# Kernel tuning notes

Measured on AMD Instinct MI355X. Metric: run time of the kernel, lower is better.

## Reference

```python
import jax, jax.numpy as jnp
import numpy as np
from itertools import product

B, D, H, W_, C = 2, 64, 64, 64, 96
OUT = 192  # c_multiplier * dim
EPS = 1e-5


def setup_inputs() -> dict:
    key = jax.random.key(0)
    k1, k2 = jax.random.split(key)
    x = jax.random.normal(k1, (B, D, H, W_, C), dtype=jnp.float32)
    ln_w = jnp.ones((8 * C,), dtype=jnp.float32)
    ln_b = jnp.zeros((8 * C,), dtype=jnp.float32)
    W = jax.random.normal(k2, (OUT, 8 * C), dtype=jnp.float32) * 0.02
    return {"x": x, "ln_w": ln_w, "ln_b": ln_b, "W": W}


def reference(x, ln_w, ln_b, W):
    # strided patch gather + concat: order matches itertools.product over (0,1)^3
    parts = [x[:, s0::2, s1::2, s2::2, :] for s0, s1, s2 in product((0, 1), repeat=3)]
    y = jnp.concatenate(parts, axis=-1)  # [B, D/2, H/2, W/2, 8C]
    # LayerNorm over last dim
    mu = jnp.mean(y, axis=-1, keepdims=True)
    var = jnp.mean(jnp.square(y - mu), axis=-1, keepdims=True)
    y = (y - mu) * jax.lax.rsqrt(var + EPS) * ln_w + ln_b
    # linear reduction (bias=False); torch Linear weight is [out, in]
    return jnp.einsum('bdhwc,oc->bdhwo', y, W)
```

## Files before the change

kernel.cpp:

```cpp
#include <hip/hip_runtime.h>
#include <stdint.h>

#define C_IN   96
#define KIN    768
#define NOUT   192
#define MTILE  32
#define LDK    776
#define EPS    1e-5f

typedef __bf16 bf16x8 __attribute__((ext_vector_type(8)));
typedef float  f32x4  __attribute__((ext_vector_type(4)));

static __device__ __forceinline__ unsigned int f2bf(float f) {
    union { float f; unsigned int u; } v; v.f = f;
    return (v.u + 0x7fffu + ((v.u >> 16) & 1u)) >> 16;
}
static __device__ __forceinline__ float bf2f(unsigned int s) {
    union { unsigned int u; float f; } v; v.u = s << 16;
    return v.f;
}
static __device__ __forceinline__ unsigned int normpack(unsigned int p, float mu, float rs) {
    float lo = (bf2f(p & 0xffffu) - mu) * rs;
    float hi = (bf2f(p >> 16)     - mu) * rs;
    return f2bf(lo) | (f2bf(hi) << 16);
}

__global__ __launch_bounds__(256) void prep_kernel(
    const float* __restrict__ W, const float* __restrict__ lnw,
    const float* __restrict__ lnb, unsigned short* __restrict__ Wb,
    float* __restrict__ bias)
{
    int o = blockIdx.x;
    int tid = threadIdx.x;
    float part = 0.f;
    for (int c = tid; c < KIN; c += 256) {
        float w = W[(size_t)o * KIN + c];
        Wb[(size_t)o * KIN + c] = (unsigned short)f2bf(w * lnw[c]);
        part += w * lnb[c];
    }
    #pragma unroll
    for (int m = 32; m >= 1; m >>= 1) part += __shfl_xor(part, m, 64);
    __shared__ float red[4];
    if ((tid & 63) == 0) red[tid >> 6] = part;
    __syncthreads();
    if (tid == 0) bias[o] = red[0] + red[1] + red[2] + red[3];
}

__global__ __launch_bounds__(256) void merge_kernel(
    const float* __restrict__ x, const unsigned short* __restrict__ Wb,
    const float* __restrict__ bias, float* __restrict__ out)
{
    __shared__ unsigned short ylds[MTILE * LDK];
    __shared__ float muL[MTILE], rsL[MTILE];

    const int tid   = threadIdx.x;
    const int tbase = blockIdx.x * MTILE;
    const int bh = blockIdx.x;
    const int h  = bh & 31;
    const int d  = (bh >> 5) & 31;
    const int b  = bh >> 10;

    const int tk = tid >> 3;
    const int i  = tid & 7;
    float sum = 0.f, sq = 0.f;
    #pragma unroll
    for (int g = 0; g < 8; ++g) {
        const int s0 = g >> 2, s1 = (g >> 1) & 1, s2 = g & 1;
        const float* src = x +
            ((size_t)((b * 64 + 2 * d + s0) * 64 + (2 * h + s1)) * 64 + (2 * tk + s2)) * C_IN;
        #pragma unroll
        for (int jj = 0; jj < 3; ++jj) {
            const int c4 = i + jj * 8;
            float4 v = *(const float4*)(src + c4 * 4);
            sum += v.x + v.y + v.z + v.w;
            sq  += v.x * v.x + v.y * v.y + v.z * v.z + v.w * v.w;
            uint2 p;
            p.x = f2bf(v.x) | (f2bf(v.y) << 16);
            p.y = f2bf(v.z) | (f2bf(v.w) << 16);
            *(uint2*)&ylds[tk * LDK + g * 96 + c4 * 4] = p;
        }
    }
    #pragma unroll
    for (int m = 4; m >= 1; m >>= 1) {
        sum += __shfl_xor(sum, m, 8);
        sq  += __shfl_xor(sq,  m, 8);
    }
    if (i == 0) {
        float mean = sum * (1.f / 768.f);
        float var  = sq * (1.f / 768.f) - mean * mean;
        muL[tk] = mean;
        rsL[tk] = rsqrtf(var + EPS);
    }
    __syncthreads();

    {
        const float mu = muL[tk], rs = rsL[tk];
        unsigned short* row = &ylds[tk * LDK + i * 96];
        #pragma unroll
        for (int jj = 0; jj < 12; ++jj) {
            uint4 u = *(const uint4*)(row + jj * 8);
            u.x = normpack(u.x, mu, rs);
            u.y = normpack(u.y, mu, rs);
            u.z = normpack(u.z, mu, rs);
            u.w = normpack(u.w, mu, rs);
            *(uint4*)(row + jj * 8) = u;
        }
    }
    __syncthreads();

    const int wv    = tid >> 6;
    const int l     = tid & 63;
    const int l15   = l & 15;
    const int quad  = l >> 4;
    const int nbase = wv * 48;
    const int koff  = quad * 8;

    f32x4 acc[2][3];
    #pragma unroll
    for (int mt = 0; mt < 2; ++mt)
        #pragma unroll
        for (int nt = 0; nt < 3; ++nt)
            acc[mt][nt] = (f32x4){0.f, 0.f, 0.f, 0.f};

    const unsigned short* arow0 = &ylds[(l15)      * LDK + koff];
    const unsigned short* arow1 = &ylds[(16 + l15) * LDK + koff];
    const unsigned short* brow0 = Wb + (size_t)(nbase +  0 + l15) * KIN + koff;
    const unsigned short* brow1 = Wb + (size_t)(nbase + 16 + l15) * KIN + koff;
    const unsigned short* brow2 = Wb + (size_t)(nbase + 32 + l15) * KIN + koff;

    #pragma unroll
    for (int kk = 0; kk < 24; ++kk) {
        const int k = kk * 32;
        bf16x8 a0 = *(const bf16x8*)(arow0 + k);
        bf16x8 a1 = *(const bf16x8*)(arow1 + k);
        bf16x8 b0 = *(const bf16x8*)(brow0 + k);
        bf16x8 b1 = *(const bf16x8*)(brow1 + k);
        bf16x8 b2 = *(const bf16x8*)(brow2 + k);
        acc[0][0] = __builtin_amdgcn_mfma_f32_16x16x32_bf16(a0, b0, acc[0][0], 0, 0, 0);
        acc[0][1] = __builtin_amdgcn_mfma_f32_16x16x32_bf16(a0, b1, acc[0][1], 0, 0, 0);
        acc[0][2] = __builtin_amdgcn_mfma_f32_16x16x32_bf16(a0, b2, acc[0][2], 0, 0, 0);
        acc[1][0] = __builtin_amdgcn_mfma_f32_16x16x32_bf16(a1, b0, acc[1][0], 0, 0, 0);
        acc[1][1] = __builtin_amdgcn_mfma_f32_16x16x32_bf16(a1, b1, acc[1][1], 0, 0, 0);
        acc[1][2] = __builtin_amdgcn_mfma_f32_16x16x32_bf16(a1, b2, acc[1][2], 0, 0, 0);
    }

    const float b0 = bias[nbase + l15];
    const float b1 = bias[nbase + 16 + l15];
    const float b2 = bias[nbase + 32 + l15];
    #pragma unroll
    for (int mt = 0; mt < 2; ++mt) {
        #pragma unroll
        for (int r = 0; r < 4; ++r) {
            const int row = mt * 16 + quad * 4 + r;
            float* op = out + (size_t)(tbase + row) * NOUT + nbase + l15;
            op[0]  = acc[mt][0][r] + b0;
            op[16] = acc[mt][1][r] + b1;
            op[32] = acc[mt][2][r] + b2;
        }
    }
}

extern "C" void kernel_launch(void* const* d_in, const int* in_sizes, int n_in,
                              void* d_out, int out_size, void* d_ws, size_t ws_size,
                              hipStream_t stream) {
    const float* x   = (const float*)d_in[0];
    const float* lnw = (const float*)d_in[1];
    const float* lnb = (const float*)d_in[2];
    const float* W   = (const float*)d_in[3];
    float* out = (float*)d_out;

    unsigned short* Wb = (unsigned short*)d_ws;
    float* bias = (float*)((char*)d_ws + (size_t)NOUT * KIN * 2);

    prep_kernel<<<NOUT, 256, 0, stream>>>(W, lnw, lnb, Wb, bias);
    merge_kernel<<<2048, 256, 0, stream>>>(x, Wb, bias, out);
}
```

Before: 345.1 us.

## Fold LayerNorm normalization into GEMM epilogue and batch global loads

```diff
diff --git a/kernel.cpp b/kernel.cpp
--- a/kernel.cpp
+++ b/kernel.cpp
@@ -5,7 +5,7 @@
 #define KIN    768
 #define NOUT   192
 #define MTILE  32
-#define LDK    776
+#define LDK    772
 #define EPS    1e-5f
 
 typedef __bf16 bf16x8 __attribute__((ext_vector_type(8)));
@@ -19,36 +19,40 @@
     union { unsigned int u; float f; } v; v.u = s << 16;
     return v.f;
 }
-static __device__ __forceinline__ unsigned int normpack(unsigned int p, float mu, float rs) {
-    float lo = (bf2f(p & 0xffffu) - mu) * rs;
-    float hi = (bf2f(p >> 16)     - mu) * rs;
-    return f2bf(lo) | (f2bf(hi) << 16);
-}
 
 __global__ __launch_bounds__(256) void prep_kernel(
     const float* __restrict__ W, const float* __restrict__ lnw,
     const float* __restrict__ lnb, unsigned short* __restrict__ Wb,
-    float* __restrict__ bias)
+    float* __restrict__ bias, float* __restrict__ Scol)
 {
     int o = blockIdx.x;
     int tid = threadIdx.x;
-    float part = 0.f;
+    float bpart = 0.f, spart = 0.f;
     for (int c = tid; c < KIN; c += 256) {
         float w = W[(size_t)o * KIN + c];
-        Wb[(size_t)o * KIN + c] = (unsigned short)f2bf(w * lnw[c]);
-        part += w * lnb[c];
+        unsigned int rb = f2bf(w * lnw[c]);
+        Wb[(size_t)o * KIN + c] = (unsigned short)rb;
+        spart += bf2f(rb);
+        bpart += w * lnb[c];
     }
     #pragma unroll
-    for (int m = 32; m >= 1; m >>= 1) part += __shfl_xor(part, m, 64);
-    __shared__ float red[4];
-    if ((tid & 63) == 0) red[tid >> 6] = part;
+    for (int m = 32; m >= 1; m >>= 1) {
+        bpart += __shfl_xor(bpart, m, 64);
+        spart += __shfl_xor(spart, m, 64);
+    }
+    __shared__ float redb[4], reds[4];
+    if ((tid & 63) == 0) { redb[tid >> 6] = bpart; reds[tid >> 6] = spart; }
     __syncthreads();
-    if (tid == 0) bias[o] = red[0] + red[1] + red[2] + red[3];
+    if (tid == 0) {
+        bias[o] = redb[0] + redb[1] + redb[2] + redb[3];
+        Scol[o] = reds[0] + reds[1] + reds[2] + reds[3];
+    }
 }
 
-__global__ __launch_bounds__(256) void merge_kernel(
+__global__ __launch_bounds__(256, 3) void merge_kernel(
     const float* __restrict__ x, const unsigned short* __restrict__ Wb,
-    const float* __restrict__ bias, float* __restrict__ out)
+    const float* __restrict__ bias, const float* __restrict__ Scol,
+    float* __restrict__ out)
 {
     __shared__ unsigned short ylds[MTILE * LDK];
     __shared__ float muL[MTILE], rsL[MTILE];
@@ -62,22 +66,30 @@
 
     const int tk = tid >> 3;
     const int i  = tid & 7;
+    const float* base = x +
+        ((size_t)((b * 64 + 2 * d) * 64 + 2 * h) * 64 + 2 * tk) * C_IN + i * 4;
+
+    const int OFF[8] = {0, 96, 6144, 6240, 393216, 393312, 399360, 399456};
+
+    float4 v[24];
+    #pragma unroll
+    for (int g = 0; g < 8; ++g)
+        #pragma unroll
+        for (int jj = 0; jj < 3; ++jj)
+            v[g * 3 + jj] = *(const float4*)(base + OFF[g] + jj * 32);
+
     float sum = 0.f, sq = 0.f;
     #pragma unroll
     for (int g = 0; g < 8; ++g) {
-        const int s0 = g >> 2, s1 = (g >> 1) & 1, s2 = g & 1;
-        const float* src = x +
-            ((size_t)((b * 64 + 2 * d + s0) * 64 + (2 * h + s1)) * 64 + (2 * tk + s2)) * C_IN;
         #pragma unroll
         for (int jj = 0; jj < 3; ++jj) {
-            const int c4 = i + jj * 8;
-            float4 v = *(const float4*)(src + c4 * 4);
-            sum += v.x + v.y + v.z + v.w;
-            sq  += v.x * v.x + v.y * v.y + v.z * v.z + v.w * v.w;
+            float4 t = v[g * 3 + jj];
+            sum += t.x + t.y + t.z + t.w;
+            sq  += t.x * t.x + t.y * t.y + t.z * t.z + t.w * t.w;
             uint2 p;
-            p.x = f2bf(v.x) | (f2bf(v.y) << 16);
-            p.y = f2bf(v.z) | (f2bf(v.w) << 16);
-            *(uint2*)&ylds[tk * LDK + g * 96 + c4 * 4] = p;
+            p.x = f2bf(t.x) | (f2bf(t.y) << 16);
+            p.y = f2bf(t.z) | (f2bf(t.w) << 16);
+            *(uint2*)&ylds[tk * LDK + g * 96 + (i + jj * 8) * 4] = p;
         }
     }
     #pragma unroll
@@ -90,21 +102,6 @@
         float var  = sq * (1.f / 768.f) - mean * mean;
         muL[tk] = mean;
         rsL[tk] = rsqrtf(var + EPS);
-    }
-    __syncthreads();
-
-    {
-        const float mu = muL[tk], rs = rsL[tk];
-        unsigned short* row = &ylds[tk * LDK + i * 96];
-        #pragma unroll
-        for (int jj = 0; jj < 12; ++jj) {
-            uint4 u = *(const uint4*)(row + jj * 8);
-            u.x = normpack(u.x, mu, rs);
-            u.y = normpack(u.y, mu, rs);
-            u.z = normpack(u.z, mu, rs);
-            u.w = normpack(u.w, mu, rs);
-            *(uint4*)(row + jj * 8) = u;
-        }
     }
     __syncthreads();
 
@@ -122,40 +119,54 @@
         for (int nt = 0; nt < 3; ++nt)
             acc[mt][nt] = (f32x4){0.f, 0.f, 0.f, 0.f};
 
-    const unsigned short* arow0 = &ylds[(l15)      * LDK + koff];
+    const unsigned short* arow0 = &ylds[l15        * LDK + koff];
     const unsigned short* arow1 = &ylds[(16 + l15) * LDK + koff];
-    const unsigned short* brow0 = Wb + (size_t)(nbase +  0 + l15) * KIN + koff;
-    const unsigned short* brow1 = Wb + (size_t)(nbase + 16 + l15) * KIN + koff;
-    const unsigned short* brow2 = Wb + (size_t)(nbase + 32 + l15) * KIN + koff;
+    const unsigned short* brow0 = Wb + (size_t)(nbase + l15) * KIN + koff;
+    const unsigned short* brow1 = brow0 + 16 * KIN;
+    const unsigned short* brow2 = brow0 + 32 * KIN;
 
+    bf16x8 a0 = *(const bf16x8*)arow0;
+    bf16x8 a1 = *(const bf16x8*)arow1;
+    bf16x8 b0 = *(const bf16x8*)brow0;
+    bf16x8 b1 = *(const bf16x8*)brow1;
+    bf16x8 b2 = *(const bf16x8*)brow2;
     #pragma unroll
     for (int kk = 0; kk < 24; ++kk) {
-        const int k = kk * 32;
-        bf16x8 a0 = *(const bf16x8*)(arow0 + k);
-        bf16x8 a1 = *(const bf16x8*)(arow1 + k);
-        bf16x8 b0 = *(const bf16x8*)(brow0 + k);
-        bf16x8 b1 = *(const bf16x8*)(brow1 + k);
-        bf16x8 b2 = *(const bf16x8*)(brow2 + k);
+        bf16x8 na0, na1, nb0, nb1, nb2;
+        if (kk < 23) {
+            const int k = (kk + 1) * 32;
+            na0 = *(const bf16x8*)(arow0 + k);
+            na1 = *(const bf16x8*)(arow1 + k);
+            nb0 = *(const bf16x8*)(brow0 + k);
+            nb1 = *(const bf16x8*)(brow1 + k);
+            nb2 = *(const bf16x8*)(brow2 + k);
+        }
         acc[0][0] = __builtin_amdgcn_mfma_f32_16x16x32_bf16(a0, b0, acc[0][0], 0, 0, 0);
         acc[0][1] = __builtin_amdgcn_mfma_f32_16x16x32_bf16(a0, b1, acc[0][1], 0, 0, 0);
         acc[0][2] = __builtin_amdgcn_mfma_f32_16x16x32_bf16(a0, b2, acc[0][2], 0, 0, 0);
         acc[1][0] = __builtin_amdgcn_mfma_f32_16x16x32_bf16(a1, b0, acc[1][0], 0, 0, 0);
         acc[1][1] = __builtin_amdgcn_mfma_f32_16x16x32_bf16(a1, b1, acc[1][1], 0, 0, 0);
         acc[1][2] = __builtin_amdgcn_mfma_f32_16x16x32_bf16(a1, b2, acc[1][2], 0, 0, 0);
+        a0 = na0; a1 = na1; b0 = nb0; b1 = nb1; b2 = nb2;
     }
 
-    const float b0 = bias[nbase + l15];
-    const float b1 = bias[nbase + 16 + l15];
-    const float b2 = bias[nbase + 32 + l15];
+    const float S0 = Scol[nbase + l15];
+    const float S1 = Scol[nbase + 16 + l15];
+    const float S2 = Scol[nbase + 32 + l15];
+    const float c0 = bias[nbase + l15];
+    const float c1 = bias[nbase + 16 + l15];
+    const float c2 = bias[nbase + 32 + l15];
     #pragma unroll
     for (int mt = 0; mt < 2; ++mt) {
         #pragma unroll
         for (int r = 0; r < 4; ++r) {
             const int row = mt * 16 + quad * 4 + r;
+            const float rs = rsL[row];
+            const float rm = rs * muL[row];
             float* op = out + (size_t)(tbase + row) * NOUT + nbase + l15;
-            op[0]  = acc[mt][0][r] + b0;
-            op[16] = acc[mt][1][r] + b1;
-            op[32] = acc[mt][2][r] + b2;
+            op[0]  = rs * acc[mt][0][r] - rm * S0 + c0;
+            op[16] = rs * acc[mt][1][r] - rm * S1 + c1;
+            op[32] = rs * acc[mt][2][r] - rm * S2 + c2;
         }
     }
 }
@@ -171,7 +182,8 @@
 
     unsigned short* Wb = (unsigned short*)d_ws;
     float* bias = (float*)((char*)d_ws + (size_t)NOUT * KIN * 2);
+    float* Scol = bias + NOUT;
 
-    prep_kernel<<<NOUT, 256, 0, stream>>>(W, lnw, lnb, Wb, bias);
-    merge_kernel<<<2048, 256, 0, stream>>>(x, Wb, bias, out);
+    prep_kernel<<<NOUT, 256, 0, stream>>>(W, lnw, lnb, Wb, bias, Scol);
+    merge_kernel<<<2048, 256, 0, stream>>>(x, Wb, bias, Scol, out);
 }
```

Measured after the change: 345.7 us. No clear change (+0.2%).
